# Performance work log

Hardware: AMD Instinct MI355X
Metric: run time of the kernel (lower is better)

The kernel has to match this reference:

```python
import jax, jax.numpy as jnp
import numpy as np

N = 8192
D_IN = 512
D_OUT = 64
ALPHA = 0.2  # LeakyReLU negative slope
MASK_VAL = -9e15


def setup_inputs() -> dict:
    key = jax.random.key(0)
    k1, k2, k3, k4 = jax.random.split(key, 4)
    inp = jax.random.normal(k1, (N, D_IN), dtype=jnp.float32)
    adj = (jax.random.uniform(k2, (N, N)) < 0.05).astype(jnp.float32)
    adj = adj.at[jnp.arange(N), jnp.arange(N)].set(1.0)
    W = jax.random.normal(k3, (D_IN, D_OUT), dtype=jnp.float32) * 0.05
    a = jax.random.normal(k4, (2 * D_OUT, 1), dtype=jnp.float32) * 0.05
    return {"input": inp, "adj": adj, "W": W, "a": a}


def reference(input, adj, W, a):
    # h = input @ W : [n, out]
    h = input @ W
    # Algebraic equivalent of the dense pairwise concat:
    # e_ij = leakyrelu([h_i || h_j] . a) = leakyrelu(h_i.a1 + h_j.a2)
    a1, a2 = a[:D_OUT, 0], a[D_OUT:, 0]          # [out], [out]
    e = jax.nn.leaky_relu(
        (h @ a1)[:, None] + (h @ a2)[None, :],    # [n, n]
        negative_slope=ALPHA,
    )
    attention = jnp.where(adj > 0, e, MASK_VAL)
    attention = jax.nn.softmax(attention, axis=1)
    out = attention @ h                            # [n, out]
    return jax.nn.elu(out)                         # end=False branch
```

## Files before the change

kernel.cpp:

```cpp
#include <hip/hip_runtime.h>
#include <hip/hip_bf16.h>

#define N 8192
#define D_IN 512
#define D_OUT 64
#define ALPHA 0.2f
#define BM 16
#define NSPLIT 4
#define KSEG (N / NSPLIT)
#define NSH (KSEG / 128)
#define MLP 260

typedef __attribute__((ext_vector_type(4))) float f32x4;
typedef __attribute__((ext_vector_type(8))) short bf16x8;

static __device__ __forceinline__ unsigned pk_bf16(float lo, float hi) {
    unsigned ulo = __bfloat16_as_ushort(__float2bfloat16(lo));
    unsigned uhi = __bfloat16_as_ushort(__float2bfloat16(hi));
    return (uhi << 16) | ulo;
}

__global__ __launch_bounds__(256) void gat_h_kernel(
    const float* __restrict__ input, const float* __restrict__ W,
    const float* __restrict__ a, unsigned short* __restrict__ hpk,
    float* __restrict__ s1, float* __restrict__ s2)
{
    __shared__ float hp[4][4][64];
    int ws   = threadIdx.x >> 6;
    int lane = threadIdx.x & 63;
    int row0 = blockIdx.x * 4;
    const float* in0 = input + (size_t)row0 * D_IN + ws * 128;
    const float* Wp  = W + ws * 128 * D_OUT;
    float acc[4] = {0.f, 0.f, 0.f, 0.f};
#pragma unroll 4
    for (int k = 0; k < 128; ++k) {
        float wk = Wp[k * D_OUT + lane];
#pragma unroll
        for (int r = 0; r < 4; ++r)
            acc[r] = fmaf(in0[r * D_IN + k], wk, acc[r]);
    }
#pragma unroll
    for (int r = 0; r < 4; ++r) hp[ws][r][lane] = acc[r];
    __syncthreads();
    if (ws == 0) {
        float h[4];
#pragma unroll
        for (int r = 0; r < 4; ++r)
            h[r] = (hp[0][r][lane] + hp[1][r][lane]) + (hp[2][r][lane] + hp[3][r][lane]);
        int kw = row0 >> 5, kb = (row0 >> 3) & 3, e0 = row0 & 7;
        int dw = lane >> 4, dd = lane & 15;
        size_t off = ((size_t)((kw * 4 + dw) * 64) + kb * 16 + dd) * 8 + e0;
        uint2 hv;
        hv.x = pk_bf16(h[0], h[1]);
        hv.y = pk_bf16(h[2], h[3]);
        *(uint2*)(hpk + off) = hv;
        float a1 = a[lane], a2 = a[D_OUT + lane];
#pragma unroll
        for (int r = 0; r < 4; ++r) {
            float p1 = h[r] * a1;
            float p2 = h[r] * a2;
#pragma unroll
            for (int off2 = 32; off2; off2 >>= 1) {
                p1 += __shfl_xor(p1, off2, 64);
                p2 += __shfl_xor(p2, off2, 64);
            }
            if (lane == 0) { s1[row0 + r] = p1; s2[row0 + r] = p2; }
        }
    }
}

struct SSP { float4 sA, sB; };
struct UBP { uint4 b0, b1, b2, b3; };

static __device__ __forceinline__ void issue_s(SSP& p, const float* sb, int ps) {
    p.sA = *(const float4*)(sb + ps * 128);
    p.sB = *(const float4*)(sb + ps * 128 + 4);
}
static __device__ __forceinline__ void issue_ub(UBP& p, const unsigned short* hb,
                                                int ps) {
    const unsigned short* f = hb + ((size_t)ps << 13);
    p.b0 = *(const uint4*)(f);
    p.b1 = *(const uint4*)(f + 512);
    p.b2 = *(const uint4*)(f + 1024);
    p.b3 = *(const uint4*)(f + 1536);
}

__global__ __launch_bounds__(256, 4) void gat_flash_kernel(
    const float* __restrict__ adj, const unsigned short* __restrict__ hpk,
    const float* __restrict__ s1, const float* __restrict__ s2,
    float* __restrict__ pacc, float* __restrict__ plsum)
{
    __shared__ unsigned char ml[BM * MLP];
    __shared__ float Cl[4][BM][D_OUT];
    __shared__ float lsl[4][BM];

    const int tid  = threadIdx.x;
    const int lane = tid & 63;
    const int ws   = tid >> 6;
    const int i    = lane & 15;
    const int kb   = lane >> 4;
    const int hf   = blockIdx.x >> 9;
    const int rb   = blockIdx.x & 511;
    const int rg   = rb * BM + i;

#pragma unroll
    for (int g = 0; g < 4; ++g) {
        int r = ws * 4 + g;
        const float* rowp = adj + (size_t)(rb * BM + r) * N + hf * KSEG + lane * 8;
        float4 v[8];
#pragma unroll
        for (int c = 0; c < 4; ++c) {
            v[2 * c]     = *(const float4*)(rowp + c * 512);
            v[2 * c + 1] = *(const float4*)(rowp + c * 512 + 4);
        }
#pragma unroll
        for (int c = 0; c < 4; ++c) {
            float4 v0 = v[2 * c], v1 = v[2 * c + 1];
            unsigned b =  (unsigned)(v0.x > 0.f)
                       | ((unsigned)(v0.y > 0.f) << 1)
                       | ((unsigned)(v0.z > 0.f) << 2)
                       | ((unsigned)(v0.w > 0.f) << 3)
                       | ((unsigned)(v1.x > 0.f) << 4)
                       | ((unsigned)(v1.y > 0.f) << 5)
                       | ((unsigned)(v1.z > 0.f) << 6)
                       | ((unsigned)(v1.w > 0.f) << 7);
            ml[r * MLP + c * 64 + lane] = (unsigned char)b;
        }
    }
    __syncthreads();

    const float* s2b = s2 + hf * KSEG + ws * 32 + kb * 8;
    const unsigned short* hb = hpk + (((size_t)(hf * 64 + ws)) << 11) + (lane << 3);
    const unsigned char* mlb = ml + i * MLP + ws * 4 + kb;

    float s1r  = s1[rg];
    float eref = s1r + s2[rg];
    eref = eref > 0.f ? eref : ALPHA * eref;
    float lsum = 0.f;
    f32x4 acc0 = {0,0,0,0}, acc1 = {0,0,0,0}, acc2 = {0,0,0,0}, acc3 = {0,0,0,0};

    auto step = [&](const SSP& p, const UBP& u, unsigned m) {
        const float* sv0 = (const float*)&p.sA;
        const float* sv1 = (const float*)&p.sB;
        float w[8];
#pragma unroll
        for (int z = 0; z < 4; ++z) {
            float e0 = s1r + sv0[z]; e0 = e0 > 0.f ? e0 : ALPHA * e0;
            float e1 = s1r + sv1[z]; e1 = e1 > 0.f ? e1 : ALPHA * e1;
            float w0 = __expf(e0 - eref);
            float w1 = __expf(e1 - eref);
            w[z]     = ((m >> z) & 1u)       ? w0 : 0.f;
            w[z + 4] = ((m >> (z + 4)) & 1u) ? w1 : 0.f;
        }
#pragma unroll
        for (int z = 0; z < 8; ++z) lsum += w[z];
        uint4 pk;
        pk.x = pk_bf16(w[0], w[1]); pk.y = pk_bf16(w[2], w[3]);
        pk.z = pk_bf16(w[4], w[5]); pk.w = pk_bf16(w[6], w[7]);
        bf16x8 A = __builtin_bit_cast(bf16x8, pk);
        acc0 = __builtin_amdgcn_mfma_f32_16x16x32_bf16(A, __builtin_bit_cast(bf16x8, u.b0), acc0, 0, 0, 0);
        acc1 = __builtin_amdgcn_mfma_f32_16x16x32_bf16(A, __builtin_bit_cast(bf16x8, u.b1), acc1, 0, 0, 0);
        acc2 = __builtin_amdgcn_mfma_f32_16x16x32_bf16(A, __builtin_bit_cast(bf16x8, u.b2), acc2, 0, 0, 0);
        acc3 = __builtin_amdgcn_mfma_f32_16x16x32_bf16(A, __builtin_bit_cast(bf16x8, u.b3), acc3, 0, 0, 0);
    };

    SSP S0, S1; UBP U0, U1;
    issue_s(S0, s2b, 0); issue_ub(U0, hb, 0);
    issue_s(S1, s2b, 1); issue_ub(U1, hb, 1);
    for (int p = 0; p < NSH; p += 2) {
        unsigned m0 = mlb[p * 16];
        step(S0, U0, m0);
        if (p + 2 < NSH) { issue_s(S0, s2b, p + 2); issue_ub(U0, hb, p + 2); }
        unsigned m1 = mlb[(p + 1) * 16];
        step(S1, U1, m1);
        if (p + 3 < NSH) { issue_s(S1, s2b, p + 3); issue_ub(U1, hb, p + 3); }
    }

    lsum += __shfl_xor(lsum, 16, 64);
    lsum += __shfl_xor(lsum, 32, 64);
    if (lane < 16) lsl[ws][lane] = lsum;

    const f32x4 av[4] = {acc0, acc1, acc2, acc3};
#pragma unroll
    for (int dw = 0; dw < 4; ++dw)
#pragma unroll
        for (int reg = 0; reg < 4; ++reg)
            Cl[ws][kb * 4 + reg][dw * 16 + i] = av[dw][reg];
    __syncthreads();

#pragma unroll
    for (int o = tid; o < BM * D_OUT; o += 256) {
        int row = o >> 6, d = o & 63;
        float v = (Cl[0][row][d] + Cl[1][row][d]) + (Cl[2][row][d] + Cl[3][row][d]);
        pacc[((size_t)hf * N + rb * BM + row) * 64 + d] = v;
    }
    if (tid < BM)
        plsum[hf * N + rb * BM + tid] =
            (lsl[0][tid] + lsl[1][tid]) + (lsl[2][tid] + lsl[3][tid]);
}

__global__ __launch_bounds__(256) void gat_reduce_kernel(
    const float* __restrict__ pacc, const float* __restrict__ plsum,
    float* __restrict__ out)
{
    int idx = blockIdx.x * 256 + threadIdx.x;
    int row = idx >> 6;
    float aa = 0.f, l = 0.f;
#pragma unroll
    for (int hf = 0; hf < NSPLIT; ++hf) {
        aa += pacc[(size_t)hf * N * 64 + idx];
        l  += plsum[hf * N + row];
    }
    float o = aa / l;
    out[idx] = o > 0.f ? o : expm1f(o);
}

extern "C" void kernel_launch(void* const* d_in, const int* in_sizes, int n_in,
                              void* d_out, int out_size, void* d_ws, size_t ws_size,
                              hipStream_t stream) {
    const float* input = (const float*)d_in[0];
    const float* adj   = (const float*)d_in[1];
    const float* W     = (const float*)d_in[2];
    const float* a     = (const float*)d_in[3];
    float* out = (float*)d_out;

    unsigned short* hpk = (unsigned short*)d_ws;
    float* s1    = (float*)(hpk + (size_t)N * D_OUT);
    float* s2    = s1 + N;
    float* pacc  = s2 + N;
    float* plsum = pacc + (size_t)NSPLIT * N * 64;

    gat_h_kernel<<<2048, 256, 0, stream>>>(input, W, a, hpk, s1, s2);
    gat_flash_kernel<<<512 * NSPLIT, 256, 0, stream>>>(adj, hpk, s1, s2, pacc, plsum);
    gat_reduce_kernel<<<N * 64 / 256, 256, 0, stream>>>(pacc, plsum, out);
}
```

Measured before the change: 118.6 us.

## Precompute adjacency bitmask in separate kernel with MFMA-friendly layout

Moves the adjacency-to-bitmask conversion out of the attention kernel into a dedicated pass that writes bytes in a layout matching each lane's access order. The attention kernel then reads packed 32-bit mask words directly from global memory instead of staging through shared memory with a barrier. The aim is to let the mask pass run at full streaming bandwidth with high occupancy, separate from the compute-heavy kernel. The cost is an extra launch plus a write and re-read of an 8 MB mask buffer.

```diff
diff --git a/kernel.cpp b/kernel.cpp
--- a/kernel.cpp
+++ b/kernel.cpp
@@ -6,10 +6,10 @@
 #define D_OUT 64
 #define ALPHA 0.2f
 #define BM 16
+#define NRB (N / BM)
 #define NSPLIT 4
 #define KSEG (N / NSPLIT)
 #define NSH (KSEG / 128)
-#define MLP 260
 
 typedef __attribute__((ext_vector_type(4))) float f32x4;
 typedef __attribute__((ext_vector_type(8))) short bf16x8;
@@ -18,6 +18,41 @@
     unsigned ulo = __bfloat16_as_ushort(__float2bfloat16(lo));
     unsigned uhi = __bfloat16_as_ushort(__float2bfloat16(hi));
     return (uhi << 16) | ulo;
+}
+
+__global__ __launch_bounds__(256) void gat_mask_kernel(
+    const float* __restrict__ adj, unsigned char* __restrict__ msk2)
+{
+    size_t wave = ((size_t)blockIdx.x * 256 + threadIdx.x) >> 6;
+    int lane = threadIdx.x & 63;
+    const float* base = adj + wave * 4096 + (size_t)lane * 8;
+    float4 v[16];
+#pragma unroll
+    for (int it = 0; it < 8; ++it) {
+        v[2 * it]     = *(const float4*)(base + it * 512);
+        v[2 * it + 1] = *(const float4*)(base + it * 512 + 4);
+    }
+#pragma unroll
+    for (int it = 0; it < 8; ++it) {
+        float4 v0 = v[2 * it], v1 = v[2 * it + 1];
+        unsigned b =  (unsigned)(v0.x > 0.f)
+                   | ((unsigned)(v0.y > 0.f) << 1)
+                   | ((unsigned)(v0.z > 0.f) << 2)
+                   | ((unsigned)(v0.w > 0.f) << 3)
+                   | ((unsigned)(v1.x > 0.f) << 4)
+                   | ((unsigned)(v1.y > 0.f) << 5)
+                   | ((unsigned)(v1.z > 0.f) << 6)
+                   | ((unsigned)(v1.w > 0.f) << 7);
+        size_t chunk = wave * 512 + (size_t)it * 64 + lane;
+        int row = (int)(chunk >> 10);
+        int cb  = (int)(chunk & 1023);
+        int hf = cb >> 8, rem = cb & 255;
+        int p = rem >> 4, ws = (rem >> 2) & 3, kb = rem & 3;
+        int q = p >> 2, j = p & 3;
+        unsigned u = ((unsigned)(row >> 4)) * 4096 + hf * 1024 + q * 256
+                   + ws * 64 + kb * 16 + (row & 15);
+        msk2[(size_t)u * 4 + j] = (unsigned char)b;
+    }
 }
 
 __global__ __launch_bounds__(256) void gat_h_kernel(
@@ -72,25 +107,11 @@
 struct SSP { float4 sA, sB; };
 struct UBP { uint4 b0, b1, b2, b3; };
 
-static __device__ __forceinline__ void issue_s(SSP& p, const float* sb, int ps) {
-    p.sA = *(const float4*)(sb + ps * 128);
-    p.sB = *(const float4*)(sb + ps * 128 + 4);
-}
-static __device__ __forceinline__ void issue_ub(UBP& p, const unsigned short* hb,
-                                                int ps) {
-    const unsigned short* f = hb + ((size_t)ps << 13);
-    p.b0 = *(const uint4*)(f);
-    p.b1 = *(const uint4*)(f + 512);
-    p.b2 = *(const uint4*)(f + 1024);
-    p.b3 = *(const uint4*)(f + 1536);
-}
-
 __global__ __launch_bounds__(256, 4) void gat_flash_kernel(
-    const float* __restrict__ adj, const unsigned short* __restrict__ hpk,
+    const unsigned char* __restrict__ msk2, const unsigned short* __restrict__ hpk,
     const float* __restrict__ s1, const float* __restrict__ s2,
     float* __restrict__ pacc, float* __restrict__ plsum)
 {
-    __shared__ unsigned char ml[BM * MLP];
     __shared__ float Cl[4][BM][D_OUT];
     __shared__ float lsl[4][BM];
 
@@ -103,35 +124,10 @@
     const int rb   = blockIdx.x & 511;
     const int rg   = rb * BM + i;
 
-#pragma unroll
-    for (int g = 0; g < 4; ++g) {
-        int r = ws * 4 + g;
-        const float* rowp = adj + (size_t)(rb * BM + r) * N + hf * KSEG + lane * 8;
-        float4 v[8];
-#pragma unroll
-        for (int c = 0; c < 4; ++c) {
-            v[2 * c]     = *(const float4*)(rowp + c * 512);
-            v[2 * c + 1] = *(const float4*)(rowp + c * 512 + 4);
-        }
-#pragma unroll
-        for (int c = 0; c < 4; ++c) {
-            float4 v0 = v[2 * c], v1 = v[2 * c + 1];
-            unsigned b =  (unsigned)(v0.x > 0.f)
-                       | ((unsigned)(v0.y > 0.f) << 1)
-                       | ((unsigned)(v0.z > 0.f) << 2)
-                       | ((unsigned)(v0.w > 0.f) << 3)
-                       | ((unsigned)(v1.x > 0.f) << 4)
-                       | ((unsigned)(v1.y > 0.f) << 5)
-                       | ((unsigned)(v1.z > 0.f) << 6)
-                       | ((unsigned)(v1.w > 0.f) << 7);
-            ml[r * MLP + c * 64 + lane] = (unsigned char)b;
-        }
-    }
-    __syncthreads();
-
+    const unsigned* mb_u = (const unsigned*)msk2
+        + (size_t)rb * 4096 + hf * 1024 + ws * 64 + lane;
     const float* s2b = s2 + hf * KSEG + ws * 32 + kb * 8;
     const unsigned short* hb = hpk + (((size_t)(hf * 64 + ws)) << 11) + (lane << 3);
-    const unsigned char* mlb = ml + i * MLP + ws * 4 + kb;
 
     float s1r  = s1[rg];
     float eref = s1r + s2[rg];
@@ -139,6 +135,17 @@
     float lsum = 0.f;
     f32x4 acc0 = {0,0,0,0}, acc1 = {0,0,0,0}, acc2 = {0,0,0,0}, acc3 = {0,0,0,0};
 
+    auto issue_s = [&](SSP& p, int ps) {
+        p.sA = *(const float4*)(s2b + ps * 128);
+        p.sB = *(const float4*)(s2b + ps * 128 + 4);
+    };
+    auto issue_u = [&](UBP& p, int ps) {
+        const unsigned short* f = hb + ((size_t)ps << 13);
+        p.b0 = *(const uint4*)(f);
+        p.b1 = *(const uint4*)(f + 512);
+        p.b2 = *(const uint4*)(f + 1024);
+        p.b3 = *(const uint4*)(f + 1536);
+    };
     auto step = [&](const SSP& p, const UBP& u, unsigned m) {
         const float* sv0 = (const float*)&p.sA;
         const float* sv1 = (const float*)&p.sB;
@@ -165,15 +172,21 @@
     };
 
     SSP S0, S1; UBP U0, U1;
-    issue_s(S0, s2b, 0); issue_ub(U0, hb, 0);
-    issue_s(S1, s2b, 1); issue_ub(U1, hb, 1);
+    issue_s(S0, 0); issue_u(U0, 0);
+    issue_s(S1, 1); issue_u(U1, 1);
+    unsigned mqc = mb_u[0];
+    unsigned mqn = mb_u[256];
     for (int p = 0; p < NSH; p += 2) {
-        unsigned m0 = mlb[p * 16];
+        if (p && (p & 3) == 0) {
+            mqc = mqn;
+            if (p < 12) mqn = mb_u[(size_t)(p / 4 + 1) * 256];
+        }
+        unsigned m0 = (mqc >> ((p & 3) * 8)) & 0xffu;
+        unsigned m1 = (mqc >> ((p & 3) * 8 + 8)) & 0xffu;
         step(S0, U0, m0);
-        if (p + 2 < NSH) { issue_s(S0, s2b, p + 2); issue_ub(U0, hb, p + 2); }
-        unsigned m1 = mlb[(p + 1) * 16];
+        if (p + 2 < NSH) { issue_s(S0, p + 2); issue_u(U0, p + 2); }
         step(S1, U1, m1);
-        if (p + 3 < NSH) { issue_s(S1, s2b, p + 3); issue_ub(U1, hb, p + 3); }
+        if (p + 3 < NSH) { issue_s(S1, p + 3); issue_u(U1, p + 3); }
     }
 
     lsum += __shfl_xor(lsum, 16, 64);
@@ -229,8 +242,10 @@
     float* s2    = s1 + N;
     float* pacc  = s2 + N;
     float* plsum = pacc + (size_t)NSPLIT * N * 64;
-
+    unsigned char* msk2 = (unsigned char*)(plsum + (size_t)NSPLIT * N);
+
+    gat_mask_kernel<<<4096, 256, 0, stream>>>(adj, msk2);
     gat_h_kernel<<<2048, 256, 0, stream>>>(input, W, a, hpk, s1, s2);
-    gat_flash_kernel<<<512 * NSPLIT, 256, 0, stream>>>(adj, hpk, s1, s2, pacc, plsum);
+    gat_flash_kernel<<<NRB * NSPLIT, 256, 0, stream>>>(msk2, hpk, s1, s2, pacc, plsum);
     gat_reduce_kernel<<<N * 64 / 256, 256, 0, stream>>>(pacc, plsum, out);
 }
```

After: 139.0 us. 1.17x slower.
